# Optimization experiments

Hardware: AMD Instinct MI355X
Metric: run time of the kernel (lower is better)

## Reference

```python
import jax, jax.numpy as jnp
import numpy as np

N = 50000
IN_DIM = 256
HID = 64
HEADS = 4
OUT_DIM = 40
E = 800000
NEG_SLOPE = 0.2


def setup_inputs() -> dict:
    key = jax.random.key(0)
    ks = jax.random.split(key, 12)
    x = jax.random.normal(ks[0], (N, IN_DIM), dtype=jnp.float32)
    edge_index = jax.random.randint(ks[1], (2, E), 0, N, dtype=jnp.int64)
    s = 0.05
    W1 = jax.random.normal(ks[2], (IN_DIM, HEADS * HID), dtype=jnp.float32) * s
    att_src1 = jax.random.normal(ks[3], (HEADS, HID), dtype=jnp.float32) * s
    att_dst1 = jax.random.normal(ks[4], (HEADS, HID), dtype=jnp.float32) * s
    b1 = jnp.zeros((HEADS * HID,), dtype=jnp.float32)
    W2 = jax.random.normal(ks[5], (HEADS * HID, OUT_DIM), dtype=jnp.float32) * s
    att_src2 = jax.random.normal(ks[6], (1, OUT_DIM), dtype=jnp.float32) * s
    att_dst2 = jax.random.normal(ks[7], (1, OUT_DIM), dtype=jnp.float32) * s
    b2 = jnp.zeros((OUT_DIM,), dtype=jnp.float32)
    return {"x": x, "edge_index": edge_index, "W1": W1, "att_src1": att_src1,
            "att_dst1": att_dst1, "b1": b1, "W2": W2, "att_src2": att_src2,
            "att_dst2": att_dst2, "b2": b2}


def _gat_conv(x, src, dst, W, a_src, a_dst, b, heads, out_ch, concat):
    n = x.shape[0]
    h = (x @ W).reshape(n, heads, out_ch)              # [N,H,C]
    alpha_s = jnp.einsum('nhc,hc->nh', h, a_src)       # [N,H]
    alpha_d = jnp.einsum('nhc,hc->nh', h, a_dst)
    e = jax.nn.leaky_relu(alpha_s[src] + alpha_d[dst], NEG_SLOPE)  # [E,H]
    # segment softmax over destination neighborhoods
    m = jax.ops.segment_max(e, dst, num_segments=n)    # [N,H]
    ex = jnp.exp(e - m[dst])
    denom = jax.ops.segment_sum(ex, dst, num_segments=n)
    alpha = ex / (denom[dst] + 1e-16)                  # [E,H]
    out = jax.ops.segment_sum(h[src] * alpha[:, :, None], dst, num_segments=n)  # [N,H,C]
    out = out.reshape(n, heads * out_ch) if concat else out.mean(axis=1)
    return out + b


def reference(x, edge_index, W1, att_src1, att_dst1, b1, W2, att_src2, att_dst2, b2):
    # PyG GATConv adds self-loops by default
    loops = jnp.arange(N, dtype=edge_index.dtype)
    src = jnp.concatenate([edge_index[0], loops])
    dst = jnp.concatenate([edge_index[1], loops])
    h = _gat_conv(x, src, dst, W1, att_src1, att_dst1, b1, HEADS, HID, True)
    h = jax.nn.elu(h)
    h = _gat_conv(h, src, dst, W2, att_src2, att_dst2, b2, 1, OUT_DIM, False)
    return jax.nn.log_softmax(h, axis=1)
```

## Files before the change

### kernel.cpp

```cpp
#include <hip/hip_runtime.h>
#include <hip/hip_bf16.h>
#include <math.h>

#define NNODES 50000
#define M_PAD  50048
#define IN_DIM 256
#define HID 64
#define HEADS 4
#define OUT_DIM 40
#define NEDGES 800000
#define ETOT (NEDGES + NNODES)
#define NEG_SLOPE 0.2f
#define MAXDEG 64
#define SCAT_CH 416
#define PREP_BLKS (307 + SCAT_CH * 8)

typedef __attribute__((ext_vector_type(8))) short bf16x8;
typedef __attribute__((ext_vector_type(4))) float f32x4;
typedef __attribute__((ext_vector_type(2))) float f32x2;
typedef unsigned char uchar;

__device__ __forceinline__ ushort f2bf(float f) {
    uint u = __float_as_uint(f);
    u += 0x7FFF + ((u >> 16) & 1);
    return (ushort)(u >> 16);
}
__device__ __forceinline__ uint fkey(float f) {
    uint u = __float_as_uint(f);
    return (u & 0x80000000u) ? ~u : (u | 0x80000000u);
}
__device__ __forceinline__ float fdec(uint k) {
    return (k & 0x80000000u) ? __uint_as_float(k & 0x7fffffffu) : __uint_as_float(~k);
}
__device__ __forceinline__ float wave_reduce_max(float v) {
    #pragma unroll
    for (int off = 32; off > 0; off >>= 1) v = fmaxf(v, __shfl_xor(v, off));
    return v;
}
__device__ __forceinline__ float wave_reduce_sum(float v) {
    #pragma unroll
    for (int off = 32; off > 0; off >>= 1) v += __shfl_xor(v, off);
    return v;
}
__device__ __forceinline__ uchar f2fp8(float v) {
    return (uchar)(__builtin_amdgcn_cvt_pk_fp8_f32(v, v, 0, false) & 0xFF);
}
__device__ __forceinline__ void accum8f8(f32x2* acc2, uint2 hv, float wgt) {
    f32x2 wv = {wgt, wgt};
    f32x2 p;
    p = __builtin_amdgcn_cvt_pk_f32_fp8(hv.x, false); acc2[0] += p * wv;
    p = __builtin_amdgcn_cvt_pk_f32_fp8(hv.x, true);  acc2[1] += p * wv;
    p = __builtin_amdgcn_cvt_pk_f32_fp8(hv.y, false); acc2[2] += p * wv;
    p = __builtin_amdgcn_cvt_pk_f32_fp8(hv.y, true);  acc2[3] += p * wv;
}
__device__ __forceinline__ float lrw(float e, float mm) {
    return __expf(fmaxf(e, NEG_SLOPE * e) - mm);
}
__device__ __forceinline__ uint dpart(int d) {
    return ((uint)d * 10737u) >> 26;
}

__global__ void prep_kernel(const float* __restrict__ W1, const float* __restrict__ W2,
                            const float* __restrict__ a2s, const float* __restrict__ a2d,
                            const int* __restrict__ ei,
                            ushort* __restrict__ W1t, ushort* __restrict__ W2tb,
                            float* __restrict__ wa_s, float* __restrict__ wa_d,
                            int* __restrict__ counts, int* __restrict__ col) {
    int b = blockIdx.x, t = threadIdx.x;
    if (b >= 307) {
        int b2 = b - 307;
        uint part = (uint)(b2 & 7);
        int chunk = b2 >> 3;
        int base = chunk * 2048 + t * 8;
        if (base >= ETOT) return;
        int s[8], d[8];
        if (base + 8 <= NEDGES) {
            int4 sa = *reinterpret_cast<const int4*>(ei + base);
            int4 sb = *reinterpret_cast<const int4*>(ei + base + 4);
            int4 da = *reinterpret_cast<const int4*>(ei + NEDGES + base);
            int4 db = *reinterpret_cast<const int4*>(ei + NEDGES + base + 4);
            s[0] = sa.x; s[1] = sa.y; s[2] = sa.z; s[3] = sa.w;
            s[4] = sb.x; s[5] = sb.y; s[6] = sb.z; s[7] = sb.w;
            d[0] = da.x; d[1] = da.y; d[2] = da.z; d[3] = da.w;
            d[4] = db.x; d[5] = db.y; d[6] = db.z; d[7] = db.w;
        } else {
            #pragma unroll
            for (int k = 0; k < 8; k++) {
                int idx = base + k;
                if (idx < NEDGES) { s[k] = ei[idx]; d[k] = ei[NEDGES + idx]; }
                else if (idx < ETOT) { s[k] = idx - NEDGES; d[k] = s[k]; }
                else { s[k] = 0; d[k] = -1; }
            }
        }
        #pragma unroll
        for (int k = 0; k < 8; k++) {
            if (d[k] >= 0 && dpart(d[k]) == part) {
                int pos = atomicAdd(&counts[d[k]], 1);
                if (pos < MAXDEG) col[d[k] * MAXDEG + pos] = s[k];
            }
        }
        return;
    }
    if (b < 256) {
        W1t[b * 256 + t] = f2bf(W1[t * 256 + b]);
    } else if (b < 306) {
        int idx = (b - 256) * 256 + t;
        if (idx < 48 * 264) {
            int n = idx / 264, k = idx % 264;
            W2tb[idx] = (n < OUT_DIM && k < 256) ? f2bf(W2[k * OUT_DIM + n]) : (ushort)0;
        }
    } else {
        float ss = 0.f, sd = 0.f;
        #pragma unroll 8
        for (int c = 0; c < OUT_DIM; c++) {
            float wv = W2[t * OUT_DIM + c];
            ss += wv * a2s[c];
            sd += wv * a2d[c];
        }
        wa_s[t] = ss;
        wa_d[t] = sd;
    }
}

__global__ __launch_bounds__(256) void gemm1_fused(const float* __restrict__ x,
                                                   const ushort* __restrict__ W1t,
                                                   const float* __restrict__ asrc,
                                                   const float* __restrict__ adst,
                                                   uchar* __restrict__ h1f8,
                                                   float* __restrict__ as1,
                                                   float* __restrict__ ad1,
                                                   uint* __restrict__ gb) {
    __shared__ ushort As[64 * 32];
    __shared__ ushort Bs[256 * 32];
    __shared__ uint smax[4];
    int t = threadIdx.x;
    int l = t & 63, wn = t >> 6;
    int m0 = blockIdx.x * 64;
    int lrow = l & 15, lks = l >> 4;
    int ks = lks ^ ((lrow >> 1) & 3);

    f32x4 acc[4][4];
    #pragma unroll
    for (int i = 0; i < 4; i++)
        #pragma unroll
        for (int j = 0; j < 4; j++) acc[i][j] = (f32x4){0.f, 0.f, 0.f, 0.f};

    for (int k0 = 0; k0 < 256; k0 += 32) {
        #pragma unroll
        for (int i = 0; i < 2; i++) {
            int idx = t + 256 * i;
            int row = idx >> 3, c4 = idx & 7;
            int grow = m0 + row;
            float4 v = make_float4(0.f, 0.f, 0.f, 0.f);
            if (grow < NNODES) v = *reinterpret_cast<const float4*>(x + (size_t)grow * 256 + k0 + c4 * 4);
            uint2 p;
            p.x = (uint)f2bf(v.x) | ((uint)f2bf(v.y) << 16);
            p.y = (uint)f2bf(v.z) | ((uint)f2bf(v.w) << 16);
            int slot = (c4 >> 1) ^ ((row >> 1) & 3);
            *reinterpret_cast<uint2*>(&As[row * 32 + slot * 8 + (c4 & 1) * 4]) = p;
        }
        #pragma unroll
        for (int i = 0; i < 4; i++) {
            int idx = t + 256 * i;
            int row = idx >> 2, skb = idx & 3;
            uint4 bv = *reinterpret_cast<const uint4*>(W1t + (size_t)row * 256 + k0 + skb * 8);
            int slot = skb ^ ((row >> 1) & 3);
            *reinterpret_cast<uint4*>(&Bs[row * 32 + slot * 8]) = bv;
        }
        __syncthreads();
        bf16x8 a_frag[4], b_frag[4];
        #pragma unroll
        for (int mf = 0; mf < 4; mf++)
            a_frag[mf] = *reinterpret_cast<const bf16x8*>(&As[(mf * 16 + lrow) * 32 + ks * 8]);
        #pragma unroll
        for (int nf = 0; nf < 4; nf++)
            b_frag[nf] = *reinterpret_cast<const bf16x8*>(&Bs[(wn * 64 + nf * 16 + lrow) * 32 + ks * 8]);
        #pragma unroll
        for (int mf = 0; mf < 4; mf++)
            #pragma unroll
            for (int nf = 0; nf < 4; nf++)
                acc[mf][nf] = __builtin_amdgcn_mfma_f32_16x16x32_bf16(a_frag[mf], b_frag[nf], acc[mf][nf], 0, 0, 0);
        __syncthreads();
    }

    #pragma unroll
    for (int mf = 0; mf < 4; mf++)
        #pragma unroll
        for (int nf = 0; nf < 4; nf++) {
            int col_ = wn * 64 + nf * 16 + lrow;
            #pragma unroll
            for (int r = 0; r < 4; r++) {
                int row = m0 + mf * 16 + lks * 4 + r;
                h1f8[(size_t)row * 256 + col_] = f2fp8(acc[mf][nf][r]);
            }
        }

    float a_s[4], a_d[4];
    #pragma unroll
    for (int nf = 0; nf < 4; nf++) {
        a_s[nf] = asrc[wn * 64 + nf * 16 + lrow];
        a_d[nf] = adst[wn * 64 + nf * 16 + lrow];
    }
    float ps[4][4], pd[4][4];
    #pragma unroll
    for (int mf = 0; mf < 4; mf++)
        #pragma unroll
        for (int r = 0; r < 4; r++) {
            float s = 0.f, d = 0.f;
            #pragma unroll
            for (int nf = 0; nf < 4; nf++) {
                s += acc[mf][nf][r] * a_s[nf];
                d += acc[mf][nf][r] * a_d[nf];
            }
            ps[mf][r] = s; pd[mf][r] = d;
        }
    #pragma unroll
    for (int off = 1; off < 16; off <<= 1)
        #pragma unroll
        for (int mf = 0; mf < 4; mf++)
            #pragma unroll
            for (int r = 0; r < 4; r++) {
                ps[mf][r] += __shfl_xor(ps[mf][r], off);
                pd[mf][r] += __shfl_xor(pd[mf][r], off);
            }
    if (lrow == 0) {
        #pragma unroll
        for (int mf = 0; mf < 4; mf++)
            #pragma unroll
            for (int r = 0; r < 4; r++) {
                int row = m0 + mf * 16 + lks * 4 + r;
                if (row < NNODES) {
                    as1[row * 4 + wn] = ps[mf][r];
                    ad1[row * 4 + wn] = pd[mf][r];
                }
            }
    }
    float vmax = -INFINITY;
    #pragma unroll
    for (int mf = 0; mf < 4; mf++)
        #pragma unroll
        for (int r = 0; r < 4; r++) {
            int row = m0 + mf * 16 + lks * 4 + r;
            if (row < NNODES) vmax = fmaxf(vmax, ps[mf][r]);
        }
    vmax = fmaxf(vmax, __shfl_xor(vmax, 16));
    vmax = fmaxf(vmax, __shfl_xor(vmax, 32));
    if (l == 0) smax[wn] = fkey(vmax);
    __syncthreads();
    if (t < 4) atomicMax(&gb[t], smax[t]);
}

__global__ __launch_bounds__(256) void agg1_kernel(const uchar* __restrict__ h1f8,
                                                   const float* __restrict__ as1,
                                                   const float* __restrict__ ad1,
                                                   const int* __restrict__ cnt,
                                                   const int* __restrict__ col,
                                                   const float* __restrict__ b1,
                                                   const uint* __restrict__ gb,
                                                   const float* __restrict__ wa_s,
                                                   const float* __restrict__ wa_d,
                                                   ushort* __restrict__ out1b,
                                                   float* __restrict__ as2,
                                                   float* __restrict__ ad2) {
    int tid = threadIdx.x;
    int lane = tid & 63, wid = tid >> 6;
    int n = blockIdx.x * 4 + wid;
    int j = lane & 31, half = lane >> 5;
    int myh = j >> 3, sub = j & 3;
    int bcast = lane & ~3;
    int deg = min(cnt[n], MAXDEG);
    const int* cp = col + n * MAXDEG;

    float adn = ad1[n * 4 + myh];
    float g = fdec(gb[myh]);
    float mt = g + adn;
    float mm = fmaxf(mt, NEG_SLOPE * mt);

    f32x2 acc2[4];
    #pragma unroll
    for (int k = 0; k < 4; k++) acc2[k] = (f32x2){0.f, 0.f};
    float ls = 0.f;
    uint jb = (uint)(j * 8);

    int done = 0;
    for (; done + 8 <= deg; done += 8) {
        const int* p = cp + done + half * 4;
        int4 ca = *reinterpret_cast<const int4*>(p);
        int sown = sub == 0 ? ca.x : sub == 1 ? ca.y : sub == 2 ? ca.z : ca.w;
        float q = as1[(uint)(sown * 4 + myh)];
        uint2 h0 = *reinterpret_cast<const uint2*>(h1f8 + (((uint)ca.x << 8) + jb));
        uint2 h1v = *reinterpret_cast<const uint2*>(h1f8 + (((uint)ca.y << 8) + jb));
        uint2 h2v = *reinterpret_cast<const uint2*>(h1f8 + (((uint)ca.z << 8) + jb));
        uint2 h3v = *reinterpret_cast<const uint2*>(h1f8 + (((uint)ca.w << 8) + jb));
        float wown = lrw(q + adn, mm);
        float w0 = __shfl(wown, bcast + 0);
        float w1 = __shfl(wown, bcast + 1);
        float w2 = __shfl(wown, bcast + 2);
        float w3 = __shfl(wown, bcast + 3);
        ls += (w0 + w1) + (w2 + w3);
        accum8f8(acc2, h0, w0);
        accum8f8(acc2, h1v, w1);
        accum8f8(acc2, h2v, w2);
        accum8f8(acc2, h3v, w3);
    }
    if (done < deg) {
        int base = done + half * 4;
        int4 ca = *reinterpret_cast<const int4*>(cp + base);
        int s0 = (base + 0 < deg) ? ca.x : 0;
        int s1 = (base + 1 < deg) ? ca.y : 0;
        int s2 = (base + 2 < deg) ? ca.z : 0;
        int s3 = (base + 3 < deg) ? ca.w : 0;
        int sown = sub == 0 ? s0 : sub == 1 ? s1 : sub == 2 ? s2 : s3;
        float q = as1[(uint)(sown * 4 + myh)];
        uint2 h0 = *reinterpret_cast<const uint2*>(h1f8 + (((uint)s0 << 8) + jb));
        uint2 h1v = *reinterpret_cast<const uint2*>(h1f8 + (((uint)s1 << 8) + jb));
        uint2 h2v = *reinterpret_cast<const uint2*>(h1f8 + (((uint)s2 << 8) + jb));
        uint2 h3v = *reinterpret_cast<const uint2*>(h1f8 + (((uint)s3 << 8) + jb));
        float wown = (base + sub < deg) ? lrw(q + adn, mm) : 0.f;
        float w0 = __shfl(wown, bcast + 0);
        float w1 = __shfl(wown, bcast + 1);
        float w2 = __shfl(wown, bcast + 2);
        float w3 = __shfl(wown, bcast + 3);
        ls += (w0 + w1) + (w2 + w3);
        accum8f8(acc2, h0, w0);
        accum8f8(acc2, h1v, w1);
        accum8f8(acc2, h2v, w2);
        accum8f8(acc2, h3v, w3);
    }
    #pragma unroll
    for (int k = 0; k < 4; k++) {
        acc2[k].x += __shfl_xor(acc2[k].x, 32);
        acc2[k].y += __shfl_xor(acc2[k].y, 32);
    }
    ls += __shfl_xor(ls, 32);

    float dinv = 1.f / (ls + 1e-16f);
    float4 bA = *reinterpret_cast<const float4*>(b1 + j * 8);
    float4 bB = *reinterpret_cast<const float4*>(b1 + j * 8 + 4);
    float4 wsA = *reinterpret_cast<const float4*>(wa_s + j * 8);
    float4 wsB = *reinterpret_cast<const float4*>(wa_s + j * 8 + 4);
    float4 wdA = *reinterpret_cast<const float4*>(wa_d + j * 8);
    float4 wdB = *reinterpret_cast<const float4*>(wa_d + j * 8 + 4);
    float o[8];
    o[0] = acc2[0].x * dinv + bA.x; o[1] = acc2[0].y * dinv + bA.y;
    o[2] = acc2[1].x * dinv + bA.z; o[3] = acc2[1].y * dinv + bA.w;
    o[4] = acc2[2].x * dinv + bB.x; o[5] = acc2[2].y * dinv + bB.y;
    o[6] = acc2[3].x * dinv + bB.z; o[7] = acc2[3].y * dinv + bB.w;
    #pragma unroll
    for (int e8 = 0; e8 < 8; e8++) o[e8] = o[e8] > 0.f ? o[e8] : expm1f(o[e8]);
    float dps = o[0] * wsA.x + o[1] * wsA.y + o[2] * wsA.z + o[3] * wsA.w
              + o[4] * wsB.x + o[5] * wsB.y + o[6] * wsB.z + o[7] * wsB.w;
    float dpd = o[0] * wdA.x + o[1] * wdA.y + o[2] * wdA.z + o[3] * wdA.w
              + o[4] * wdB.x + o[5] * wdB.y + o[6] * wdB.z + o[7] * wdB.w;
    #pragma unroll
    for (int off = 1; off < 32; off <<= 1) {
        dps += __shfl_xor(dps, off);
        dpd += __shfl_xor(dpd, off);
    }
    if (lane == 0) { as2[n] = dps; ad2[n] = dpd; }
    if (lane < 32) {
        uint4 pk;
        pk.x = (uint)f2bf(o[0]) | ((uint)f2bf(o[1]) << 16);
        pk.y = (uint)f2bf(o[2]) | ((uint)f2bf(o[3]) << 16);
        pk.z = (uint)f2bf(o[4]) | ((uint)f2bf(o[5]) << 16);
        pk.w = (uint)f2bf(o[6]) | ((uint)f2bf(o[7]) << 16);
        *reinterpret_cast<uint4*>(out1b + ((uint)n * 256 + (uint)j * 8)) = pk;
    }
}

__global__ __launch_bounds__(256) void gemm2_kernel(const ushort* __restrict__ Ag,
                                                    const ushort* __restrict__ Bg,
                                                    const float* __restrict__ as2,
                                                    uchar* __restrict__ h2f8,
                                                    uint* __restrict__ gb) {
    __shared__ ushort Bs[48 * 264];
    int t = threadIdx.x;
    int l = t & 63, w = t >> 6;
    int lrow = l & 15, lks = l >> 4;
    for (int idx = t; idx < 48 * 264 / 8; idx += 256)
        reinterpret_cast<uint4*>(Bs)[idx] = reinterpret_cast<const uint4*>(Bg)[idx];
    __syncthreads();

    int m0 = blockIdx.x * 64 + w * 16;
    f32x4 acc[3];
    #pragma unroll
    for (int nf = 0; nf < 3; nf++) acc[nf] = (f32x4){0.f, 0.f, 0.f, 0.f};

    #pragma unroll
    for (int k0 = 0; k0 < 256; k0 += 32) {
        bf16x8 af = *reinterpret_cast<const bf16x8*>(Ag + (size_t)(m0 + lrow) * 256 + k0 + lks * 8);
        #pragma unroll
        for (int nf = 0; nf < 3; nf++) {
            bf16x8 bf = *reinterpret_cast<const bf16x8*>(&Bs[(nf * 16 + lrow) * 264 + k0 + lks * 8]);
            acc[nf] = __builtin_amdgcn_mfma_f32_16x16x32_bf16(af, bf, acc[nf], 0, 0, 0);
        }
    }
    #pragma unroll
    for (int nf = 0; nf < 3; nf++) {
        int c = nf * 16 + lrow;
        if (c < OUT_DIM) {
            #pragma unroll
            for (int r = 0; r < 4; r++) {
                int row = m0 + lks * 4 + r;
                if (row < NNODES) h2f8[(size_t)row * OUT_DIM + c] = f2fp8(acc[nf][r]);
            }
        }
    }
    if (t < 64) {
        int row = blockIdx.x * 64 + t;
        float v = (row < NNODES) ? as2[row] : -INFINITY;
        v = wave_reduce_max(v);
        if (t == 0) atomicMax(&gb[4], fkey(v));
    }
}

__global__ __launch_bounds__(256) void agg2_kernel(const uchar* __restrict__ h2f8,
                                                   const float* __restrict__ as2,
                                                   const float* __restrict__ ad2,
                                                   const int* __restrict__ cnt,
                                                   const int* __restrict__ col,
                                                   const float* __restrict__ b2,
                                                   const uint* __restrict__ gb,
                                                   float* __restrict__ out) {
    int tid = threadIdx.x;
    int lane = tid & 63, wid = tid >> 6;
    int n = blockIdx.x * 4 + wid;
    int j = lane & 31, half = lane >> 5;
    int sub = j & 3;
    int bcast = lane & ~3;
    int deg = min(cnt[n], MAXDEG);
    const int* cp = col + n * MAXDEG;
    float adn = ad2[n];
    float g = fdec(gb[4]);
    float mt = g + adn;
    float mm = fmaxf(mt, NEG_SLOPE * mt);

    bool act = j < 20;
    uint jo = (uint)(j * 2);
    f32x2 a2 = {0.f, 0.f};
    float ls = 0.f;

    int done = 0;
    for (; done + 8 <= deg; done += 8) {
        const int* p = cp + done + half * 4;
        int4 ca = *reinterpret_cast<const int4*>(p);
        int sown = sub == 0 ? ca.x : sub == 1 ? ca.y : sub == 2 ? ca.z : ca.w;
        float q = as2[(uint)sown];
        uint v0 = 0, v1 = 0, v2 = 0, v3 = 0;
        if (act) {
            v0 = *reinterpret_cast<const ushort*>(h2f8 + ((uint)ca.x * 40 + jo));
            v1 = *reinterpret_cast<const ushort*>(h2f8 + ((uint)ca.y * 40 + jo));
            v2 = *reinterpret_cast<const ushort*>(h2f8 + ((uint)ca.z * 40 + jo));
            v3 = *reinterpret_cast<const ushort*>(h2f8 + ((uint)ca.w * 40 + jo));
        }
        float wown = lrw(q + adn, mm);
        float w0 = __shfl(wown, bcast + 0);
        float w1 = __shfl(wown, bcast + 1);
        float w2 = __shfl(wown, bcast + 2);
        float w3 = __shfl(wown, bcast + 3);
        ls += (w0 + w1) + (w2 + w3);
        a2 += __builtin_amdgcn_cvt_pk_f32_fp8(v0, false) * (f32x2){w0, w0};
        a2 += __builtin_amdgcn_cvt_pk_f32_fp8(v1, false) * (f32x2){w1, w1};
        a2 += __builtin_amdgcn_cvt_pk_f32_fp8(v2, false) * (f32x2){w2, w2};
        a2 += __builtin_amdgcn_cvt_pk_f32_fp8(v3, false) * (f32x2){w3, w3};
    }
    if (done < deg) {
        int base = done + half * 4;
        int4 ca = *reinterpret_cast<const int4*>(cp + base);
        int s0 = (base + 0 < deg) ? ca.x : 0;
        int s1 = (base + 1 < deg) ? ca.y : 0;
        int s2 = (base + 2 < deg) ? ca.z : 0;
        int s3 = (base + 3 < deg) ? ca.w : 0;
        int sown = sub == 0 ? s0 : sub == 1 ? s1 : sub == 2 ? s2 : s3;
        float q = as2[(uint)sown];
        uint v0 = 0, v1 = 0, v2 = 0, v3 = 0;
        if (act) {
            v0 = *reinterpret_cast<const ushort*>(h2f8 + ((uint)s0 * 40 + jo));
            v1 = *reinterpret_cast<const ushort*>(h2f8 + ((uint)s1 * 40 + jo));
            v2 = *reinterpret_cast<const ushort*>(h2f8 + ((uint)s2 * 40 + jo));
            v3 = *reinterpret_cast<const ushort*>(h2f8 + ((uint)s3 * 40 + jo));
        }
        float wown = (base + sub < deg) ? lrw(q + adn, mm) : 0.f;
        float w0 = __shfl(wown, bcast + 0);
        float w1 = __shfl(wown, bcast + 1);
        float w2 = __shfl(wown, bcast + 2);
        float w3 = __shfl(wown, bcast + 3);
        ls += (w0 + w1) + (w2 + w3);
        a2 += __builtin_amdgcn_cvt_pk_f32_fp8(v0, false) * (f32x2){w0, w0};
        a2 += __builtin_amdgcn_cvt_pk_f32_fp8(v1, false) * (f32x2){w1, w1};
        a2 += __builtin_amdgcn_cvt_pk_f32_fp8(v2, false) * (f32x2){w2, w2};
        a2 += __builtin_amdgcn_cvt_pk_f32_fp8(v3, false) * (f32x2){w3, w3};
    }
    a2.x += __shfl_xor(a2.x, 32);
    a2.y += __shfl_xor(a2.y, 32);
    ls += __shfl_xor(ls, 32);

    bool lead = lane < 20;
    float v0 = -INFINITY, v1 = -INFINITY;
    if (lead) {
        float2 bb = *reinterpret_cast<const float2*>(b2 + 2 * j);
        float dinv = 1.f / (ls + 1e-16f);
        v0 = a2.x * dinv + bb.x;
        v1 = a2.y * dinv + bb.y;
    }
    float mx = wave_reduce_max(fmaxf(v0, v1));
    float es = lead ? (__expf(v0 - mx) + __expf(v1 - mx)) : 0.f;
    float ssum = wave_reduce_sum(es);
    float lg = logf(ssum);
    if (lead) {
        float2 o2 = make_float2(v0 - mx - lg, v1 - mx - lg);
        *reinterpret_cast<float2*>(out + (size_t)n * OUT_DIM + 2 * j) = o2;
    }
}

extern "C" void kernel_launch(void* const* d_in, const int* in_sizes, int n_in,
                              void* d_out, int out_size, void* d_ws, size_t ws_size,
                              hipStream_t stream) {
    const float* x        = (const float*)d_in[0];
    const int*   ei       = (const int*)d_in[1];
    const float* W1       = (const float*)d_in[2];
    const float* att_src1 = (const float*)d_in[3];
    const float* att_dst1 = (const float*)d_in[4];
    const float* b1       = (const float*)d_in[5];
    const float* W2       = (const float*)d_in[6];
    const float* att_src2 = (const float*)d_in[7];
    const float* att_dst2 = (const float*)d_in[8];
    const float* b2       = (const float*)d_in[9];
    float* out = (float*)d_out;

    char* ws = (char*)d_ws;
    auto alloc = [&](size_t bytes) {
        char* p = ws;
        ws += (bytes + 255) & ~(size_t)255;
        return p;
    };
    uchar*  h1f8   = (uchar*)alloc((size_t)M_PAD * 256);
    ushort* out1b  = (ushort*)alloc((size_t)M_PAD * 256 * 2);
    ushort* W1t    = (ushort*)alloc((size_t)256 * 256 * 2);
    ushort* W2tb   = (ushort*)alloc((size_t)48 * 264 * 2);
    uchar*  h2f8   = (uchar*)alloc((size_t)M_PAD * OUT_DIM);
    float*  as1    = (float*)alloc((size_t)NNODES * 4 * 4);
    float*  ad1    = (float*)alloc((size_t)NNODES * 4 * 4);
    float*  as2    = (float*)alloc((size_t)NNODES * 4);
    float*  ad2    = (float*)alloc((size_t)NNODES * 4);
    float*  wa_s   = (float*)alloc((size_t)256 * 4);
    float*  wa_d   = (float*)alloc((size_t)256 * 4);
    int*    counts = (int*)alloc((size_t)(NNODES + 8) * 4);
    uint*   gmaxb  = (uint*)(counts + NNODES);
    int*    col    = (int*)alloc((size_t)NNODES * MAXDEG * 4);
    if ((size_t)(ws - (char*)d_ws) > ws_size) return;

    hipMemsetAsync(counts, 0, (size_t)(NNODES + 8) * 4, stream);

    prep_kernel<<<PREP_BLKS, 256, 0, stream>>>(W1, W2, att_src2, att_dst2, ei,
                                               W1t, W2tb, wa_s, wa_d, counts, col);

    gemm1_fused<<<M_PAD / 64, 256, 0, stream>>>(x, W1t, att_src1, att_dst1,
                                                h1f8, as1, ad1, gmaxb);
    agg1_kernel<<<NNODES / 4, 256, 0, stream>>>(h1f8, as1, ad1, counts, col, b1, gmaxb,
                                                wa_s, wa_d, out1b, as2, ad2);
    gemm2_kernel<<<M_PAD / 64, 256, 0, stream>>>(out1b, W2tb, as2, h2f8, gmaxb);
    agg2_kernel<<<NNODES / 4, 256, 0, stream>>>(h2f8, as2, ad2, counts, col, b2, gmaxb, out);
}
```

Measured before the change: 174.5 us.

## Fuse edge-list CSR scatter into first GEMM kernel, shrink prep kernel

```diff
diff --git a/kernel.cpp b/kernel.cpp
--- a/kernel.cpp
+++ b/kernel.cpp
@@ -12,8 +12,9 @@
 #define ETOT (NEDGES + NNODES)
 #define NEG_SLOPE 0.2f
 #define MAXDEG 64
-#define SCAT_CH 416
-#define PREP_BLKS (307 + SCAT_CH * 8)
+#define G1_BLKS 784
+#define GEMM_ACT 782
+#define CHUNK_E 8704
 
 typedef __attribute__((ext_vector_type(8))) short bf16x8;
 typedef __attribute__((ext_vector_type(4))) float f32x4;
@@ -60,47 +61,15 @@
     return ((uint)d * 10737u) >> 26;
 }
 
-__global__ void prep_kernel(const float* __restrict__ W1, const float* __restrict__ W2,
-                            const float* __restrict__ a2s, const float* __restrict__ a2d,
-                            const int* __restrict__ ei,
-                            ushort* __restrict__ W1t, ushort* __restrict__ W2tb,
-                            float* __restrict__ wa_s, float* __restrict__ wa_d,
-                            int* __restrict__ counts, int* __restrict__ col) {
+__global__ __launch_bounds__(256) void prep_kernel(const float* __restrict__ W1,
+                                                   const float* __restrict__ W2,
+                                                   const float* __restrict__ a2s,
+                                                   const float* __restrict__ a2d,
+                                                   ushort* __restrict__ W1t,
+                                                   ushort* __restrict__ W2tb,
+                                                   float* __restrict__ wa_s,
+                                                   float* __restrict__ wa_d) {
     int b = blockIdx.x, t = threadIdx.x;
-    if (b >= 307) {
-        int b2 = b - 307;
-        uint part = (uint)(b2 & 7);
-        int chunk = b2 >> 3;
-        int base = chunk * 2048 + t * 8;
-        if (base >= ETOT) return;
-        int s[8], d[8];
-        if (base + 8 <= NEDGES) {
-            int4 sa = *reinterpret_cast<const int4*>(ei + base);
-            int4 sb = *reinterpret_cast<const int4*>(ei + base + 4);
-            int4 da = *reinterpret_cast<const int4*>(ei + NEDGES + base);
-            int4 db = *reinterpret_cast<const int4*>(ei + NEDGES + base + 4);
-            s[0] = sa.x; s[1] = sa.y; s[2] = sa.z; s[3] = sa.w;
-            s[4] = sb.x; s[5] = sb.y; s[6] = sb.z; s[7] = sb.w;
-            d[0] = da.x; d[1] = da.y; d[2] = da.z; d[3] = da.w;
-            d[4] = db.x; d[5] = db.y; d[6] = db.z; d[7] = db.w;
-        } else {
-            #pragma unroll
-            for (int k = 0; k < 8; k++) {
-                int idx = base + k;
-                if (idx < NEDGES) { s[k] = ei[idx]; d[k] = ei[NEDGES + idx]; }
-                else if (idx < ETOT) { s[k] = idx - NEDGES; d[k] = s[k]; }
-                else { s[k] = 0; d[k] = -1; }
-            }
-        }
-        #pragma unroll
-        for (int k = 0; k < 8; k++) {
-            if (d[k] >= 0 && dpart(d[k]) == part) {
-                int pos = atomicAdd(&counts[d[k]], 1);
-                if (pos < MAXDEG) col[d[k] * MAXDEG + pos] = s[k];
-            }
-        }
-        return;
-    }
     if (b < 256) {
         W1t[b * 256 + t] = f2bf(W1[t * 256 + b]);
     } else if (b < 306) {
@@ -126,14 +95,36 @@
                                                    const ushort* __restrict__ W1t,
                                                    const float* __restrict__ asrc,
                                                    const float* __restrict__ adst,
+                                                   const int* __restrict__ ei,
                                                    uchar* __restrict__ h1f8,
                                                    float* __restrict__ as1,
                                                    float* __restrict__ ad1,
-                                                   uint* __restrict__ gb) {
+                                                   uint* __restrict__ gb,
+                                                   int* __restrict__ counts,
+                                                   int* __restrict__ col) {
+    int t = threadIdx.x;
+    {
+        uint part = (uint)(blockIdx.x & 7);
+        int cbase = (int)(blockIdx.x >> 3) * CHUNK_E;
+        #pragma unroll 2
+        for (int i = 0; i < 34; i++) {
+            int idx = cbase + i * 256 + t;
+            if (idx < ETOT) {
+                int s, d;
+                if (idx < NEDGES) { s = ei[idx]; d = ei[NEDGES + idx]; }
+                else { s = idx - NEDGES; d = s; }
+                if (dpart(d) == part) {
+                    int pos = atomicAdd(&counts[d], 1);
+                    if (pos < MAXDEG) col[d * MAXDEG + pos] = s;
+                }
+            }
+        }
+    }
+    if (blockIdx.x >= GEMM_ACT) return;
+
     __shared__ ushort As[64 * 32];
     __shared__ ushort Bs[256 * 32];
     __shared__ uint smax[4];
-    int t = threadIdx.x;
     int l = t & 63, wn = t >> 6;
     int m0 = blockIdx.x * 64;
     int lrow = l & 15, lks = l >> 4;
@@ -347,7 +338,7 @@
     o[4] = acc2[2].x * dinv + bB.x; o[5] = acc2[2].y * dinv + bB.y;
     o[6] = acc2[3].x * dinv + bB.z; o[7] = acc2[3].y * dinv + bB.w;
     #pragma unroll
-    for (int e8 = 0; e8 < 8; e8++) o[e8] = o[e8] > 0.f ? o[e8] : expm1f(o[e8]);
+    for (int e8 = 0; e8 < 8; e8++) o[e8] = o[e8] > 0.f ? o[e8] : (__expf(o[e8]) - 1.f);
     float dps = o[0] * wsA.x + o[1] * wsA.y + o[2] * wsA.z + o[3] * wsA.w
               + o[4] * wsB.x + o[5] * wsB.y + o[6] * wsB.z + o[7] * wsB.w;
     float dpd = o[0] * wdA.x + o[1] * wdA.y + o[2] * wdA.z + o[3] * wdA.w
@@ -552,11 +543,12 @@
 
     hipMemsetAsync(counts, 0, (size_t)(NNODES + 8) * 4, stream);
 
-    prep_kernel<<<PREP_BLKS, 256, 0, stream>>>(W1, W2, att_src2, att_dst2, ei,
-                                               W1t, W2tb, wa_s, wa_d, counts, col);
-
-    gemm1_fused<<<M_PAD / 64, 256, 0, stream>>>(x, W1t, att_src1, att_dst1,
-                                                h1f8, as1, ad1, gmaxb);
+    prep_kernel<<<307, 256, 0, stream>>>(W1, W2, att_src2, att_dst2,
+                                         W1t, W2tb, wa_s, wa_d);
+
+    gemm1_fused<<<G1_BLKS, 256, 0, stream>>>(x, W1t, att_src1, att_dst1, ei,
+                                             h1f8, as1, ad1, gmaxb, counts, col);
+
     agg1_kernel<<<NNODES / 4, 256, 0, stream>>>(h1f8, as1, ad1, counts, col, b1, gmaxb,
                                                 wa_s, wa_d, out1b, as2, ad2);
     gemm2_kernel<<<M_PAD / 64, 256, 0, stream>>>(out1b, W2tb, as2, h2f8, gmaxb);
```

New measurement: 183.8 us. 5.3% more time.
